# Kernel optimization log

Hardware: AMD Instinct MI355X
Metric: run time of the kernel (lower is better)

Reference implementation:

```python
import jax, jax.numpy as jnp
import numpy as np

B, C, H, W = 32, 256, 64, 64
K = 32

def setup_inputs() -> dict:
    key = jax.random.key(0)
    k1, k2, k3 = jax.random.split(key, 3)
    x = jax.random.normal(k1, (B, C, H, W), dtype=jnp.float32)
    codewords = jax.random.normal(k2, (K, C), dtype=jnp.float32)
    scale = jax.random.normal(k3, (K,), dtype=jnp.float32)
    return {"x": x, "codewords": codewords, "scale": scale}

def reference(x, codewords, scale):
    Bb, Cc, Hh, Ww = x.shape
    # features: [B, N, C] with N = H*W
    features = x.reshape(Bb, Cc, Hh * Ww).transpose(0, 2, 1)
    # Euclidean cdist via ||f||^2 + ||c||^2 - 2 f.c  -> [B, N, K]
    f2 = jnp.sum(features * features, axis=-1, keepdims=True)       # [B,N,1]
    c2 = jnp.sum(codewords * codewords, axis=-1)                     # [K]
    fc = jnp.einsum('bnc,kc->bnk', features, codewords)              # [B,N,K]
    dist = jnp.sqrt(jnp.maximum(f2 + c2[None, None, :] - 2.0 * fc, 0.0))
    # softmax over codewords with per-code scale
    assignment = jax.nn.softmax(-dist * scale[None, None, :], axis=2)  # [B,N,K]
    # encoded[b,k,c] = sum_n a[b,n,k] * (f[b,n,c] - cw[k,c])
    # factored to avoid materializing the [B,N,K,C] residual tensor
    enc = jnp.einsum('bnk,bnc->bkc', assignment, features)
    a_sum = jnp.sum(assignment, axis=1)                              # [B,K]
    encoded = enc - a_sum[:, :, None] * codewords[None, :, :]        # [B,K,C]
    return encoded.mean(axis=1)                                      # [B,C]
```

## Files before the change

### kernel.cpp

```cpp
#include <hip/hip_runtime.h>
#include <hip/hip_bf16.h>
#include <math.h>

#define B_DIM 32
#define C_DIM 256
#define K_DIM 32
#define N_DIM 4096
#define NSLICE 16
#define RS 66

typedef short v8s __attribute__((ext_vector_type(8)));
typedef float v4f __attribute__((ext_vector_type(4)));

#define WS_C2    0
#define WS_CWB   32
#define WS_SPART 4128
#define WS_APART 135200

__global__ void ce_prep(const float* __restrict__ cw, float* __restrict__ ws) {
    const int j = threadIdx.x;
    unsigned short* cwb = (unsigned short*)(ws + WS_CWB);
    #pragma unroll
    for (int r = 0; r < K_DIM; ++r) {
        int idx = r * C_DIM + j;
        union { __hip_bfloat16 h; unsigned short u; } cv;
        cv.h = __float2bfloat16(cw[idx]);
        cwb[idx] = cv.u;
    }
    if (j < K_DIM) {
        float s = 0.f;
        for (int cc = 0; cc < C_DIM; ++cc) {
            float v = cw[j * C_DIM + cc];
            s = fmaf(v, v, s);
        }
        ws[WS_C2 + j] = s;
    }
}

__global__ __launch_bounds__(256, 2)
void ce_main(const float* __restrict__ x,
             const float* __restrict__ scale,
             const float* __restrict__ ws_ro,
             float* __restrict__ Spart,
             float* __restrict__ a_part) {
    __shared__ float buf[2][4][16 * RS];
    __shared__ float sA[4][C_DIM];
    __shared__ float awv[4][K_DIM];
    __shared__ float f2s[4][64];

    const int tid   = threadIdx.x;
    const int wave  = tid >> 6;
    const int lane  = tid & 63;
    const int g     = lane >> 4;
    const int m     = lane & 15;
    const int slice = blockIdx.x;
    const int b     = blockIdx.y;

    const float* xw   = x + (size_t)b * C_DIM * N_DIM + slice * 256 + wave * 64;
    const uint4* cwb4 = (const uint4*)(ws_ro + WS_CWB);
    const float* c2p  = ws_ro + WS_C2;

    float* b0 = &buf[0][wave][0];
    float* b1 = &buf[1][wave][0];

    v4f acc[2][4];
    #pragma unroll
    for (int u = 0; u < 2; ++u)
        #pragma unroll
        for (int t = 0; t < 4; ++t) acc[u][t] = (v4f){0.f, 0.f, 0.f, 0.f};

    float f2 = 0.f;
    float sLo[8], sHi[8];
    float fA[16], fB[16];

    uint4 af0 = cwb4[m * 32 + g];
    uint4 af1 = cwb4[(16 + m) * 32 + g];

    #pragma unroll
    for (int i = 0; i < 16; ++i) {
        fA[i] = xw[(size_t)(2 * i) * N_DIM + lane];
        fB[i] = xw[(size_t)(2 * i + 1) * N_DIM + lane];
    }
    #pragma unroll
    for (int i = 0; i < 16; ++i) {
        f2 = fmaf(fA[i], fA[i], f2);
        f2 = fmaf(fB[i], fB[i], f2);
        union { __hip_bfloat16 h; unsigned short u; } lo, hi;
        lo.h = __float2bfloat16(fA[i]);
        hi.h = __float2bfloat16(fB[i]);
        ((unsigned*)b0)[i * RS + lane] = ((unsigned)hi.u << 16) | lo.u;
    }

    #pragma unroll
    for (int s = 0; s < 8; ++s) {
        float* cb = (s & 1) ? b1 : b0;
        float* nb = (s & 1) ? b0 : b1;

        uint4 naf0, naf1;
        if (s < 7) {
            naf0 = cwb4[m * 32 + 4 * (s + 1) + g];
            naf1 = cwb4[(16 + m) * 32 + 4 * (s + 1) + g];
            #pragma unroll
            for (int i = 0; i < 16; ++i) {
                fA[i] = xw[(size_t)(32 * (s + 1) + 2 * i) * N_DIM + lane];
                fB[i] = xw[(size_t)(32 * (s + 1) + 2 * i + 1) * N_DIM + lane];
            }
        }

        #pragma unroll
        for (int t = 0; t < 4; ++t) {
            union { unsigned d[4]; v8s v; } fb;
            #pragma unroll
            for (int h = 0; h < 4; ++h)
                fb.d[h] = ((const unsigned*)cb)[(4 * g + h) * RS + 16 * t + m];
            union { uint4 u; v8s v; } a0, a1;
            a0.u = af0; a1.u = af1;
            acc[0][t] = __builtin_amdgcn_mfma_f32_16x16x32_bf16(a0.v, fb.v, acc[0][t], 0, 0, 0);
            acc[1][t] = __builtin_amdgcn_mfma_f32_16x16x32_bf16(a1.v, fb.v, acc[1][t], 0, 0, 0);
        }

        {
            float aLo = 0.f, aHi = 0.f;
            #pragma unroll
            for (int q = 0; q < 8; ++q) {
                uint2 w = ((const uint2*)cb)[33 * m + 8 * g + q];
                aLo += __uint_as_float(w.x << 16) + __uint_as_float(w.y << 16);
                aHi += __uint_as_float(w.x & 0xffff0000u) + __uint_as_float(w.y & 0xffff0000u);
            }
            aLo += __shfl_xor(aLo, 16); aLo += __shfl_xor(aLo, 32);
            aHi += __shfl_xor(aHi, 16); aHi += __shfl_xor(aHi, 32);
            sLo[s] = aLo; sHi[s] = aHi;
        }

        if (s < 7) {
            #pragma unroll
            for (int i = 0; i < 16; ++i) {
                f2 = fmaf(fA[i], fA[i], f2);
                f2 = fmaf(fB[i], fB[i], f2);
                union { __hip_bfloat16 h; unsigned short u; } lo, hi;
                lo.h = __float2bfloat16(fA[i]);
                hi.h = __float2bfloat16(fB[i]);
                ((unsigned*)nb)[i * RS + lane] = ((unsigned)hi.u << 16) | lo.u;
            }
            af0 = naf0; af1 = naf1;
        }
    }

    f2s[wave][lane] = f2;

    float c2v[2][4], scv[2][4];
    #pragma unroll
    for (int u = 0; u < 2; ++u)
        #pragma unroll
        for (int r = 0; r < 4; ++r) {
            int k = 16 * u + 4 * g + r;
            c2v[u][r] = c2p[k];
            scv[u][r] = scale[k];
        }

    float aacc[2][4] = {{0.f,0.f,0.f,0.f},{0.f,0.f,0.f,0.f}};
    #pragma unroll
    for (int t = 0; t < 4; ++t) {
        float f2t = f2s[wave][16 * t + m];
        float L[2][4];
        float mx = -1e30f;
        #pragma unroll
        for (int u = 0; u < 2; ++u)
            #pragma unroll
            for (int r = 0; r < 4; ++r) {
                float d2 = f2t + c2v[u][r] - 2.f * acc[u][t][r];
                float dist = sqrtf(fmaxf(d2, 0.f));
                float Lv = -dist * scv[u][r];
                L[u][r] = Lv;
                mx = fmaxf(mx, Lv);
            }
        mx = fmaxf(mx, __shfl_xor(mx, 16));
        mx = fmaxf(mx, __shfl_xor(mx, 32));
        float e[2][4], ss = 0.f;
        #pragma unroll
        for (int u = 0; u < 2; ++u)
            #pragma unroll
            for (int r = 0; r < 4; ++r) {
                e[u][r] = __expf(L[u][r] - mx);
                ss += e[u][r];
            }
        ss += __shfl_xor(ss, 16);
        ss += __shfl_xor(ss, 32);
        float inv = 1.f / ss;
        #pragma unroll
        for (int u = 0; u < 2; ++u)
            #pragma unroll
            for (int r = 0; r < 4; ++r)
                aacc[u][r] = fmaf(e[u][r], inv, aacc[u][r]);
    }

    #pragma unroll
    for (int u = 0; u < 2; ++u)
        #pragma unroll
        for (int r = 0; r < 4; ++r) {
            float v = aacc[u][r];
            v += __shfl_xor(v, 1);
            v += __shfl_xor(v, 2);
            v += __shfl_xor(v, 4);
            v += __shfl_xor(v, 8);
            if (m == 0) awv[wave][16 * u + 4 * g + r] = v;
        }

    if (g == 0) {
        #pragma unroll
        for (int s = 0; s < 8; ++s) {
            sA[wave][32 * s + 2 * m]     = sLo[s];
            sA[wave][32 * s + 2 * m + 1] = sHi[s];
        }
    }
    __syncthreads();

    float Ssum = sA[0][tid] + sA[1][tid] + sA[2][tid] + sA[3][tid];
    Spart[((size_t)b * NSLICE + slice) * C_DIM + tid] = Ssum;
    if (tid < K_DIM)
        a_part[((size_t)b * NSLICE + slice) * K_DIM + tid] =
            awv[0][tid] + awv[1][tid] + awv[2][tid] + awv[3][tid];
}

__global__ void ce_final(float* __restrict__ out,
                         const float* __restrict__ cw,
                         const float* __restrict__ Spart,
                         const float* __restrict__ a_part) {
    __shared__ float asum[K_DIM];
    const int b = blockIdx.x;
    const int c = threadIdx.x;

    if (c < K_DIM) {
        float a = 0.f;
        #pragma unroll
        for (int s = 0; s < NSLICE; ++s)
            a += a_part[((size_t)b * NSLICE + s) * K_DIM + c];
        asum[c] = a;
    }
    __syncthreads();

    float S = 0.f;
    #pragma unroll
    for (int s = 0; s < NSLICE; ++s)
        S += Spart[((size_t)b * NSLICE + s) * C_DIM + c];

    float acc2 = 0.f;
    #pragma unroll
    for (int k = 0; k < K_DIM; ++k)
        acc2 = fmaf(asum[k], cw[k * C_DIM + c], acc2);
    out[b * C_DIM + c] = (S - acc2) * (1.0f / (float)K_DIM);
}

extern "C" void kernel_launch(void* const* d_in, const int* in_sizes, int n_in,
                              void* d_out, int out_size, void* d_ws, size_t ws_size,
                              hipStream_t stream) {
    const float* x     = (const float*)d_in[0];
    const float* cw    = (const float*)d_in[1];
    const float* scale = (const float*)d_in[2];
    float* out = (float*)d_out;
    float* ws  = (float*)d_ws;

    ce_prep<<<1, 256, 0, stream>>>(cw, ws);

    dim3 grid(NSLICE, B_DIM);
    ce_main<<<grid, 256, 0, stream>>>(x, scale, ws,
                                      ws + WS_SPART, ws + WS_APART);

    ce_final<<<B_DIM, 256, 0, stream>>>(out, cw,
                                        ws + WS_SPART, ws + WS_APART);
}
```

Before: 45.00 us.

## Split channel reduction across wave pairs and double grid slices

The main kernel now gives each block 128 spatial positions instead of 256, and pairs waves so each wave in a pair covers half the 256 channels. Partial MFMA dot products are combined through shared memory, and each wave handles half the softmax tiles. This doubles the grid, shortens each wave's serial chain, and raises the occupancy hint from 2 to 4 blocks per CU. Separately, the prep kernel now runs one 64-thread block per codeword with vectorised loads and a shuffle reduction instead of a single serial block. In exchange it adds an extra LDS exchange with barriers and twice as many partial sums for the final kernel to reduce.

After: 52.27 us. 1.16x slower.

```diff
diff --git a/kernel.cpp b/kernel.cpp
--- a/kernel.cpp
+++ b/kernel.cpp
@@ -6,7 +6,7 @@
 #define C_DIM 256
 #define K_DIM 32
 #define N_DIM 4096
-#define NSLICE 16
+#define NSLICE 32
 #define RS 66
 
 typedef short v8s __attribute__((ext_vector_type(8)));
@@ -15,50 +15,59 @@
 #define WS_C2    0
 #define WS_CWB   32
 #define WS_SPART 4128
-#define WS_APART 135200
-
-__global__ void ce_prep(const float* __restrict__ cw, float* __restrict__ ws) {
-    const int j = threadIdx.x;
+#define WS_APART 266272
+
+__global__ __launch_bounds__(64)
+void ce_prep(const float* __restrict__ cw, float* __restrict__ ws) {
+    const int k    = blockIdx.x;
+    const int lane = threadIdx.x;
+    float4 v = ((const float4*)(cw + (size_t)k * C_DIM))[lane];
+    union { unsigned short s[4]; uint2 d; } o;
+    union { __hip_bfloat16 h; unsigned short u; } cv;
+    cv.h = __float2bfloat16(v.x); o.s[0] = cv.u;
+    cv.h = __float2bfloat16(v.y); o.s[1] = cv.u;
+    cv.h = __float2bfloat16(v.z); o.s[2] = cv.u;
+    cv.h = __float2bfloat16(v.w); o.s[3] = cv.u;
     unsigned short* cwb = (unsigned short*)(ws + WS_CWB);
-    #pragma unroll
-    for (int r = 0; r < K_DIM; ++r) {
-        int idx = r * C_DIM + j;
-        union { __hip_bfloat16 h; unsigned short u; } cv;
-        cv.h = __float2bfloat16(cw[idx]);
-        cwb[idx] = cv.u;
-    }
-    if (j < K_DIM) {
-        float s = 0.f;
-        for (int cc = 0; cc < C_DIM; ++cc) {
-            float v = cw[j * C_DIM + cc];
-            s = fmaf(v, v, s);
-        }
-        ws[WS_C2 + j] = s;
-    }
-}
-
-__global__ __launch_bounds__(256, 2)
+    ((uint2*)(cwb + (size_t)k * C_DIM))[lane] = o.d;
+
+    float sq = 0.f;
+    sq = fmaf(v.x, v.x, sq); sq = fmaf(v.y, v.y, sq);
+    sq = fmaf(v.z, v.z, sq); sq = fmaf(v.w, v.w, sq);
+    sq += __shfl_xor(sq, 1);
+    sq += __shfl_xor(sq, 2);
+    sq += __shfl_xor(sq, 4);
+    sq += __shfl_xor(sq, 8);
+    sq += __shfl_xor(sq, 16);
+    sq += __shfl_xor(sq, 32);
+    if (lane == 0) ws[WS_C2 + k] = sq;
+}
+
+__global__ __launch_bounds__(256, 4)
 void ce_main(const float* __restrict__ x,
              const float* __restrict__ scale,
              const float* __restrict__ ws_ro,
              float* __restrict__ Spart,
              float* __restrict__ a_part) {
     __shared__ float buf[2][4][16 * RS];
-    __shared__ float sA[4][C_DIM];
+    __shared__ float sA[4][128];
     __shared__ float awv[4][K_DIM];
     __shared__ float f2s[4][64];
 
     const int tid   = threadIdx.x;
     const int wave  = tid >> 6;
     const int lane  = tid & 63;
+    const int p     = wave >> 1;
+    const int hh    = wave & 1;
     const int g     = lane >> 4;
     const int m     = lane & 15;
     const int slice = blockIdx.x;
     const int b     = blockIdx.y;
 
-    const float* xw   = x + (size_t)b * C_DIM * N_DIM + slice * 256 + wave * 64;
+    const float* xw   = x + (size_t)b * C_DIM * N_DIM + slice * 128 + p * 64;
     const uint4* cwb4 = (const uint4*)(ws_ro + WS_CWB);
     const float* c2p  = ws_ro + WS_C2;
+    const int cbase   = hh << 7;
 
     float* b0 = &buf[0][wave][0];
     float* b1 = &buf[1][wave][0];
@@ -70,16 +79,16 @@
         for (int t = 0; t < 4; ++t) acc[u][t] = (v4f){0.f, 0.f, 0.f, 0.f};
 
     float f2 = 0.f;
-    float sLo[8], sHi[8];
+    float sLo[4], sHi[4];
     float fA[16], fB[16];
 
-    uint4 af0 = cwb4[m * 32 + g];
-    uint4 af1 = cwb4[(16 + m) * 32 + g];
+    uint4 af0 = cwb4[m * 32 + 16 * hh + g];
+    uint4 af1 = cwb4[(16 + m) * 32 + 16 * hh + g];
 
     #pragma unroll
     for (int i = 0; i < 16; ++i) {
-        fA[i] = xw[(size_t)(2 * i) * N_DIM + lane];
-        fB[i] = xw[(size_t)(2 * i + 1) * N_DIM + lane];
+        fA[i] = xw[(size_t)(cbase + 2 * i) * N_DIM + lane];
+        fB[i] = xw[(size_t)(cbase + 2 * i + 1) * N_DIM + lane];
     }
     #pragma unroll
     for (int i = 0; i < 16; ++i) {
@@ -92,18 +101,18 @@
     }
 
     #pragma unroll
-    for (int s = 0; s < 8; ++s) {
+    for (int s = 0; s < 4; ++s) {
         float* cb = (s & 1) ? b1 : b0;
         float* nb = (s & 1) ? b0 : b1;
 
         uint4 naf0, naf1;
-        if (s < 7) {
-            naf0 = cwb4[m * 32 + 4 * (s + 1) + g];
-            naf1 = cwb4[(16 + m) * 32 + 4 * (s + 1) + g];
+        if (s < 3) {
+            naf0 = cwb4[m * 32 + 16 * hh + 4 * (s + 1) + g];
+            naf1 = cwb4[(16 + m) * 32 + 16 * hh + 4 * (s + 1) + g];
             #pragma unroll
             for (int i = 0; i < 16; ++i) {
-                fA[i] = xw[(size_t)(32 * (s + 1) + 2 * i) * N_DIM + lane];
-                fB[i] = xw[(size_t)(32 * (s + 1) + 2 * i + 1) * N_DIM + lane];
+                fA[i] = xw[(size_t)(cbase + 32 * (s + 1) + 2 * i) * N_DIM + lane];
+                fB[i] = xw[(size_t)(cbase + 32 * (s + 1) + 2 * i + 1) * N_DIM + lane];
             }
         }
 
@@ -111,8 +120,8 @@
         for (int t = 0; t < 4; ++t) {
             union { unsigned d[4]; v8s v; } fb;
             #pragma unroll
-            for (int h = 0; h < 4; ++h)
-                fb.d[h] = ((const unsigned*)cb)[(4 * g + h) * RS + 16 * t + m];
+            for (int h2 = 0; h2 < 4; ++h2)
+                fb.d[h2] = ((const unsigned*)cb)[(4 * g + h2) * RS + 16 * t + m];
             union { uint4 u; v8s v; } a0, a1;
             a0.u = af0; a1.u = af1;
             acc[0][t] = __builtin_amdgcn_mfma_f32_16x16x32_bf16(a0.v, fb.v, acc[0][t], 0, 0, 0);
@@ -132,7 +141,7 @@
             sLo[s] = aLo; sHi[s] = aHi;
         }
 
-        if (s < 7) {
+        if (s < 3) {
             #pragma unroll
             for (int i = 0; i < 16; ++i) {
                 f2 = fmaf(fA[i], fA[i], f2);
@@ -146,7 +155,27 @@
         }
     }
 
+    __syncthreads();
+
+    float* comb = &buf[0][0][0];
+    #pragma unroll
+    for (int u = 0; u < 2; ++u)
+        #pragma unroll
+        for (int d = 0; d < 2; ++d) {
+            int t = 2 * (1 - hh) + d;
+            #pragma unroll
+            for (int r = 0; r < 4; ++r)
+                comb[((((p * 4 + t) * 2 + u) * 4 + r) << 6) + lane] = acc[u][t][r];
+        }
     f2s[wave][lane] = f2;
+    if (g == 0) {
+        #pragma unroll
+        for (int s = 0; s < 4; ++s) {
+            sA[wave][32 * s + 2 * m]     = sLo[s];
+            sA[wave][32 * s + 2 * m + 1] = sHi[s];
+        }
+    }
+    __syncthreads();
 
     float c2v[2][4], scv[2][4];
     #pragma unroll
@@ -160,15 +189,18 @@
 
     float aacc[2][4] = {{0.f,0.f,0.f,0.f},{0.f,0.f,0.f,0.f}};
     #pragma unroll
-    for (int t = 0; t < 4; ++t) {
-        float f2t = f2s[wave][16 * t + m];
+    for (int d = 0; d < 2; ++d) {
+        const int t = 2 * hh + d;
+        float f2t = f2s[2 * p][16 * t + m] + f2s[2 * p + 1][16 * t + m];
         float L[2][4];
         float mx = -1e30f;
         #pragma unroll
         for (int u = 0; u < 2; ++u)
             #pragma unroll
             for (int r = 0; r < 4; ++r) {
-                float d2 = f2t + c2v[u][r] - 2.f * acc[u][t][r];
+                float dv = acc[u][t][r] +
+                           comb[((((p * 4 + t) * 2 + u) * 4 + r) << 6) + lane];
+                float d2 = f2t + c2v[u][r] - 2.f * dv;
                 float dist = sqrtf(fmaxf(d2, 0.f));
                 float Lv = -dist * scv[u][r];
                 L[u][r] = Lv;
@@ -205,18 +237,10 @@
             v += __shfl_xor(v, 8);
             if (m == 0) awv[wave][16 * u + 4 * g + r] = v;
         }
-
-    if (g == 0) {
-        #pragma unroll
-        for (int s = 0; s < 8; ++s) {
-            sA[wave][32 * s + 2 * m]     = sLo[s];
-            sA[wave][32 * s + 2 * m + 1] = sHi[s];
-        }
-    }
-    __syncthreads();
-
-    float Ssum = sA[0][tid] + sA[1][tid] + sA[2][tid] + sA[3][tid];
-    Spart[((size_t)b * NSLICE + slice) * C_DIM + tid] = Ssum;
+    __syncthreads();
+
+    const int ch = tid >> 7, cl = tid & 127;
+    Spart[((size_t)b * NSLICE + slice) * C_DIM + tid] = sA[ch][cl] + sA[2 + ch][cl];
     if (tid < K_DIM)
         a_part[((size_t)b * NSLICE + slice) * K_DIM + tid] =
             awv[0][tid] + awv[1][tid] + awv[2][tid] + awv[3][tid];
@@ -260,7 +284,7 @@
     float* out = (float*)d_out;
     float* ws  = (float*)d_ws;
 
-    ce_prep<<<1, 256, 0, stream>>>(cw, ws);
+    ce_prep<<<K_DIM, 64, 0, stream>>>(cw, ws);
 
     dim3 grid(NSLICE, B_DIM);
     ce_main<<<grid, 256, 0, stream>>>(x, scale, ws,
```

## Deepen x prefetch to two stages and parallelize codeword prep across blocks

Applied to the files above, without the earlier changes.

The main kernel now double-buffers the per-slice x register loads, so loads for stage s+2 are issued while stage s is computed. This gives more memory latency hiding on a bandwidth-bound stream, at the cost of 32 extra registers per thread, which may hurt occupancy under launch_bounds(256,2). The prep kernel is also spread over 32 blocks with vectorized float4 loads and a wave-shuffle reduction for the codeword norms, replacing a single-block serial loop.

New measurement: 46.57 us. 3.5% more time.

```diff
diff --git a/kernel.cpp b/kernel.cpp
--- a/kernel.cpp
+++ b/kernel.cpp
@@ -17,24 +17,30 @@
 #define WS_SPART 4128
 #define WS_APART 135200
 
-__global__ void ce_prep(const float* __restrict__ cw, float* __restrict__ ws) {
-    const int j = threadIdx.x;
+__global__ __launch_bounds__(64)
+void ce_prep(const float* __restrict__ cw, float* __restrict__ ws) {
+    const int k    = blockIdx.x;
+    const int lane = threadIdx.x;
+    float4 v = ((const float4*)(cw + (size_t)k * C_DIM))[lane];
+    union { unsigned short s[4]; uint2 d; } o;
+    union { __hip_bfloat16 h; unsigned short u; } cv;
+    cv.h = __float2bfloat16(v.x); o.s[0] = cv.u;
+    cv.h = __float2bfloat16(v.y); o.s[1] = cv.u;
+    cv.h = __float2bfloat16(v.z); o.s[2] = cv.u;
+    cv.h = __float2bfloat16(v.w); o.s[3] = cv.u;
     unsigned short* cwb = (unsigned short*)(ws + WS_CWB);
-    #pragma unroll
-    for (int r = 0; r < K_DIM; ++r) {
-        int idx = r * C_DIM + j;
-        union { __hip_bfloat16 h; unsigned short u; } cv;
-        cv.h = __float2bfloat16(cw[idx]);
-        cwb[idx] = cv.u;
-    }
-    if (j < K_DIM) {
-        float s = 0.f;
-        for (int cc = 0; cc < C_DIM; ++cc) {
-            float v = cw[j * C_DIM + cc];
-            s = fmaf(v, v, s);
-        }
-        ws[WS_C2 + j] = s;
-    }
+    ((uint2*)(cwb + (size_t)k * C_DIM))[lane] = o.d;
+
+    float sq = 0.f;
+    sq = fmaf(v.x, v.x, sq); sq = fmaf(v.y, v.y, sq);
+    sq = fmaf(v.z, v.z, sq); sq = fmaf(v.w, v.w, sq);
+    sq += __shfl_xor(sq, 1);
+    sq += __shfl_xor(sq, 2);
+    sq += __shfl_xor(sq, 4);
+    sq += __shfl_xor(sq, 8);
+    sq += __shfl_xor(sq, 16);
+    sq += __shfl_xor(sq, 32);
+    if (lane == 0) ws[WS_C2 + k] = sq;
 }
 
 __global__ __launch_bounds__(256, 2)
@@ -71,24 +77,29 @@
 
     float f2 = 0.f;
     float sLo[8], sHi[8];
-    float fA[16], fB[16];
+    float fA[2][16], fB[2][16];
 
     uint4 af0 = cwb4[m * 32 + g];
     uint4 af1 = cwb4[(16 + m) * 32 + g];
 
     #pragma unroll
     for (int i = 0; i < 16; ++i) {
-        fA[i] = xw[(size_t)(2 * i) * N_DIM + lane];
-        fB[i] = xw[(size_t)(2 * i + 1) * N_DIM + lane];
+        fA[0][i] = xw[(size_t)(2 * i) * N_DIM + lane];
+        fB[0][i] = xw[(size_t)(2 * i + 1) * N_DIM + lane];
     }
     #pragma unroll
     for (int i = 0; i < 16; ++i) {
-        f2 = fmaf(fA[i], fA[i], f2);
-        f2 = fmaf(fB[i], fB[i], f2);
+        f2 = fmaf(fA[0][i], fA[0][i], f2);
+        f2 = fmaf(fB[0][i], fB[0][i], f2);
         union { __hip_bfloat16 h; unsigned short u; } lo, hi;
-        lo.h = __float2bfloat16(fA[i]);
-        hi.h = __float2bfloat16(fB[i]);
+        lo.h = __float2bfloat16(fA[0][i]);
+        hi.h = __float2bfloat16(fB[0][i]);
         ((unsigned*)b0)[i * RS + lane] = ((unsigned)hi.u << 16) | lo.u;
+    }
+    #pragma unroll
+    for (int i = 0; i < 16; ++i) {
+        fA[1][i] = xw[(size_t)(32 + 2 * i) * N_DIM + lane];
+        fB[1][i] = xw[(size_t)(32 + 2 * i + 1) * N_DIM + lane];
     }
 
     #pragma unroll
@@ -100,11 +111,12 @@
         if (s < 7) {
             naf0 = cwb4[m * 32 + 4 * (s + 1) + g];
             naf1 = cwb4[(16 + m) * 32 + 4 * (s + 1) + g];
-            #pragma unroll
-            for (int i = 0; i < 16; ++i) {
-                fA[i] = xw[(size_t)(32 * (s + 1) + 2 * i) * N_DIM + lane];
-                fB[i] = xw[(size_t)(32 * (s + 1) + 2 * i + 1) * N_DIM + lane];
-            }
+        }
+
+        if (s < 6) {
+            #pragma unroll
+            for (int i = 0; i < 16; ++i)
+                fA[s & 1][i] = xw[(size_t)(32 * (s + 2) + 2 * i) * N_DIM + lane];
         }
 
         #pragma unroll
@@ -132,14 +144,21 @@
             sLo[s] = aLo; sHi[s] = aHi;
         }
 
+        if (s < 6) {
+            #pragma unroll
+            for (int i = 0; i < 16; ++i)
+                fB[s & 1][i] = xw[(size_t)(32 * (s + 2) + 2 * i + 1) * N_DIM + lane];
+        }
+
         if (s < 7) {
+            const int p = (s + 1) & 1;
             #pragma unroll
             for (int i = 0; i < 16; ++i) {
-                f2 = fmaf(fA[i], fA[i], f2);
-                f2 = fmaf(fB[i], fB[i], f2);
+                f2 = fmaf(fA[p][i], fA[p][i], f2);
+                f2 = fmaf(fB[p][i], fB[p][i], f2);
                 union { __hip_bfloat16 h; unsigned short u; } lo, hi;
-                lo.h = __float2bfloat16(fA[i]);
-                hi.h = __float2bfloat16(fB[i]);
+                lo.h = __float2bfloat16(fA[p][i]);
+                hi.h = __float2bfloat16(fB[p][i]);
                 ((unsigned*)nb)[i * RS + lane] = ((unsigned)hi.u << 16) | lo.u;
             }
             af0 = naf0; af1 = naf1;
@@ -260,7 +279,7 @@
     float* out = (float*)d_out;
     float* ws  = (float*)d_ws;
 
-    ce_prep<<<1, 256, 0, stream>>>(cw, ws);
+    ce_prep<<<K_DIM, 64, 0, stream>>>(cw, ws);
 
     dim3 grid(NSLICE, B_DIM);
     ce_main<<<grid, 256, 0, stream>>>(x, scale, ws,
```
